# Kernel tuning notes

Measured on AMD Instinct MI355X. Metric: run time of the kernel, lower is better.

The kernel has to match this reference:

```python
import jax, jax.numpy as jnp
import numpy as np

N = 8192        # number of nodes (adjacency is N x N)
F_IN = 256      # in_features
F_OUT = 256     # out_features


def setup_inputs() -> dict:
    key = jax.random.key(0)
    k_x, k_adj, k_kernel, k_bias, k_beta = jax.random.split(key, 5)
    x = jax.random.normal(k_x, (N, F_IN), dtype=jnp.float32)
    adj = jax.random.uniform(k_adj, (N, N), dtype=jnp.float32)  # dense non-negative adjacency buffer
    # xavier-uniform-like scale for the kernel
    limit = float(np.sqrt(6.0 / (F_IN + F_OUT)))
    kernel = jax.random.uniform(k_kernel, (F_IN, F_OUT), dtype=jnp.float32, minval=-limit, maxval=limit)
    bias = 0.01 * jax.random.normal(k_bias, (F_OUT,), dtype=jnp.float32)
    beta = 0.01 * jax.random.normal(k_beta, (N,), dtype=jnp.float32)
    return {"x": x, "adj": adj, "kernel": kernel, "bias": bias, "beta": beta}


def reference(x, adj, kernel, bias, beta):
    # Original: diag(1/(rowsum(adj)+beta)) @ (adj + diag(beta)) @ x @ kernel + bias
    # Fused form: row-scale and diagonal-add applied without materializing NxN diag matrices.
    scale = jnp.reciprocal(jnp.sum(adj, axis=1) + beta)          # [N]
    agg = adj @ x + beta[:, None] * x                             # (adj + diag(beta)) @ x  -> [N, F_IN]
    return (scale[:, None] * agg) @ kernel + bias                 # [N, F_OUT]
```

## Files before the change

### kernel.cpp

```cpp
#include <hip/hip_runtime.h>
#include <hip/hip_bf16.h>


typedef __attribute__((ext_vector_type(8))) short  short8;
typedef __attribute__((ext_vector_type(4))) float  floatx4;

#define N_NODES 8192
#define F_DIM   256

#define ASYNC16(g, l)                                                          \
  __builtin_amdgcn_global_load_lds(                                           \
      (const __attribute__((address_space(1))) void*)(g),                     \
      (__attribute__((address_space(3))) void*)(l), 16, 0, 0)

__device__ __forceinline__ unsigned short f2bf(float f) {
  unsigned u = __float_as_uint(f);
  return (unsigned short)((u + 0x7FFFu + ((u >> 16) & 1u)) >> 16);
}

__device__ __forceinline__ short8 pack_bf16x8(floatx4 a, floatx4 b) {
  short8 r;
  r[0] = (short)f2bf(a.x);
  r[1] = (short)f2bf(a.y);
  r[2] = (short)f2bf(a.z);
  r[3] = (short)f2bf(a.w);
  r[4] = (short)f2bf(b.x);
  r[5] = (short)f2bf(b.y);
  r[6] = (short)f2bf(b.z);
  r[7] = (short)f2bf(b.w);
  return r;
}

__global__ __launch_bounds__(256) void tile_bf16_kernel(
    const float* __restrict__ src, unsigned short* __restrict__ dst, int K) {
  const int Nn = F_DIM;
  int cid = blockIdx.x * 256 + threadIdx.x;
  int per_kblk = Nn * 4;
  int kblk = cid / per_kblk;
  int rem  = cid - kblk * per_kblk;
  int n16 = rem >> 6;
  int kg  = (rem >> 4) & 3;
  int nl  = rem & 15;
  int n = n16 * 16 + nl;
  int k = kblk * 32 + kg * 8;
  const float* s = src + (size_t)k * Nn + n;
  floatx4 v0, v1;
  v0.x = s[0];
  v0.y = s[(size_t)Nn];
  v0.z = s[(size_t)2 * Nn];
  v0.w = s[(size_t)3 * Nn];
  v1.x = s[(size_t)4 * Nn];
  v1.y = s[(size_t)5 * Nn];
  v1.z = s[(size_t)6 * Nn];
  v1.w = s[(size_t)7 * Nn];
  *(short8*)(dst + (size_t)cid * 8) = pack_bf16x8(v0, v1);
}

template <int KS>
__global__ __launch_bounds__(256, 2) void stage1_kernel(
    const float* __restrict__ adj, const unsigned short* __restrict__ xbt,
    float* __restrict__ part, float* __restrict__ rsp) {
  __shared__ float         At[64 * 32];
  __shared__ unsigned short Bt[32 * F_DIM];

  const int tid = threadIdx.x;
  const int w  = tid >> 6;
  const int l  = tid & 63;
  const int kq = l >> 4;
  const int ml = l & 15;
  const int m0 = blockIdx.x * 64;
  const int ks = blockIdx.y;
  const int kbeg   = ks * (N_NODES / KS);
  const int KSTEPS = (N_NODES / KS) / 32;

  const int arow = w * 16 + (l >> 3);
  const int srcg = (l & 7) ^ ((l >> 3) & 7);
  const float* agp0 = adj + (size_t)(m0 + arow) * N_NODES + kbeg + srcg * 4;
  const float* agp1 = agp0 + (size_t)8 * N_NODES;
  float* aldst0 = At + (w * 2) * 256;
  float* aldst1 = At + (w * 2 + 1) * 256;
  const unsigned short* bgp =
      xbt + (size_t)(kbeg / 32) * (32 * F_DIM) + (w * 4) * 512 + l * 8;
  unsigned short* bldst = Bt + (w * 4) * 512;

  int aoff0[4], aoff1[4], boff[4];
#pragma unroll
  for (int mf = 0; mf < 4; ++mf) {
    int m = mf * 16 + ml;
    aoff0[mf] = m * 32 + (((kq * 2)     ^ (m & 7)) * 4);
    aoff1[mf] = m * 32 + (((kq * 2 + 1) ^ (m & 7)) * 4);
  }
#pragma unroll
  for (int nf = 0; nf < 4; ++nf)
    boff[nf] = (w * 4 + nf) * 512 + kq * 128 + ml * 8;

  floatx4 acc[4][4];
  const floatx4 zf4 = {0.f, 0.f, 0.f, 0.f};
#pragma unroll
  for (int mf = 0; mf < 4; ++mf)
#pragma unroll
    for (int nf = 0; nf < 4; ++nf) acc[mf][nf] = zf4;
  float rsum[4] = {0.f, 0.f, 0.f, 0.f};

  for (int s = 0; s < KSTEPS; ++s) {
    ASYNC16(agp0, aldst0);
    ASYNC16(agp1, aldst1);
    ASYNC16(bgp,         bldst);
    ASYNC16(bgp +  512,  bldst +  512);
    ASYNC16(bgp + 1024,  bldst + 1024);
    ASYNC16(bgp + 1536,  bldst + 1536);
    agp0 += 32; agp1 += 32; bgp += 32 * F_DIM;
    __syncthreads();

    short8 af[4];
#pragma unroll
    for (int mf = 0; mf < 4; ++mf) {
      floatx4 a0 = *(const floatx4*)(At + aoff0[mf]);
      floatx4 a1 = *(const floatx4*)(At + aoff1[mf]);
      if (w == 0)
        rsum[mf] += (a0.x + a0.y + a0.z + a0.w) + (a1.x + a1.y + a1.z + a1.w);
      af[mf] = pack_bf16x8(a0, a1);
    }
#pragma unroll
    for (int nf = 0; nf < 4; ++nf) {
      short8 bv = *(const short8*)(Bt + boff[nf]);
#pragma unroll
      for (int mf = 0; mf < 4; ++mf)
        acc[mf][nf] =
            __builtin_amdgcn_mfma_f32_16x16x32_bf16(af[mf], bv, acc[mf][nf], 0, 0, 0);
    }
    __syncthreads();
  }

  float* pout = part + (size_t)ks * N_NODES * F_DIM;
#pragma unroll
  for (int mf = 0; mf < 4; ++mf)
#pragma unroll
    for (int nf = 0; nf < 4; ++nf) {
      int col = w * 64 + nf * 16 + ml;
#pragma unroll
      for (int r = 0; r < 4; ++r) {
        int row = m0 + mf * 16 + kq * 4 + r;
        pout[(size_t)row * F_DIM + col] = acc[mf][nf][r];
      }
    }

  if (w == 0) {
#pragma unroll
    for (int mf = 0; mf < 4; ++mf) {
      float v = rsum[mf];
      v += __shfl_xor(v, 16);
      v += __shfl_xor(v, 32);
      if (kq == 0) rsp[ks * N_NODES + m0 + mf * 16 + ml] = v;
    }
  }
}

template <int KS>
__global__ __launch_bounds__(256, 2) void stage2_kernel(
    const float* part, const float* __restrict__ rsp,
    const float* __restrict__ x, const float* __restrict__ beta,
    const float* __restrict__ bias, const unsigned short* __restrict__ wbt,
    float* out) {
  __shared__ unsigned short At[32 * 32];
  __shared__ unsigned short Bt[32 * F_DIM];
  __shared__ float sscale[32];
  __shared__ float sbeta[32];

  const int tid = threadIdx.x;
  const int w  = tid >> 6;
  const int l  = tid & 63;
  const int kq = l >> 4;
  const int ml = l & 15;
  const int m0 = blockIdx.x * 32;

  if (tid < 32) {
    float rs = 0.f;
#pragma unroll
    for (int p = 0; p < KS; ++p) rs += rsp[p * N_NODES + m0 + tid];
    float b = beta[m0 + tid];
    sbeta[tid]  = b;
    sscale[tid] = 1.0f / (rs + b);
  }
  __syncthreads();

  floatx4 acc[2][4];
  const floatx4 zf4 = {0.f, 0.f, 0.f, 0.f};
#pragma unroll
  for (int mf = 0; mf < 2; ++mf)
#pragma unroll
    for (int nf = 0; nf < 4; ++nf) acc[mf][nf] = zf4;

  const unsigned short* bgp = wbt + (w * 4) * 512 + l * 8;
  unsigned short* bldst = Bt + (w * 4) * 512;

  for (int s = 0; s < 8; ++s) {
    ASYNC16(bgp,        bldst);
    ASYNC16(bgp +  512, bldst +  512);
    ASYNC16(bgp + 1024, bldst + 1024);
    ASYNC16(bgp + 1536, bldst + 1536);
    bgp += 32 * F_DIM;

    if (tid < 128) {
      int r = tid >> 2, g = tid & 3;
      size_t off = (size_t)(m0 + r) * F_DIM + s * 32 + g * 8;
      floatx4 v0 = *(const floatx4*)(x + off);
      floatx4 v1 = *(const floatx4*)(x + off + 4);
      float bb = sbeta[r];
      v0 *= bb; v1 *= bb;
#pragma unroll
      for (int p = 0; p < KS; ++p) {
        const float* pp = part + (size_t)p * N_NODES * F_DIM + off;
        v0 += *(const floatx4*)pp;
        v1 += *(const floatx4*)(pp + 4);
      }
      float sc = sscale[r];
      v0 *= sc; v1 *= sc;
      *(short8*)(At + r * 32 + ((g ^ (r & 3)) * 8)) = pack_bf16x8(v0, v1);
    }
    __syncthreads();

    short8 af[2];
#pragma unroll
    for (int mf = 0; mf < 2; ++mf) {
      int m = mf * 16 + ml;
      af[mf] = *(const short8*)(At + m * 32 + ((kq ^ (m & 3)) * 8));
    }
#pragma unroll
    for (int nf = 0; nf < 4; ++nf) {
      short8 bv = *(const short8*)(Bt + (w * 4 + nf) * 512 + kq * 128 + ml * 8);
#pragma unroll
      for (int mf = 0; mf < 2; ++mf)
        acc[mf][nf] =
            __builtin_amdgcn_mfma_f32_16x16x32_bf16(af[mf], bv, acc[mf][nf], 0, 0, 0);
    }
    __syncthreads();
  }

#pragma unroll
  for (int nf = 0; nf < 4; ++nf) {
    int col = w * 64 + nf * 16 + ml;
    float bv = bias[col];
#pragma unroll
    for (int mf = 0; mf < 2; ++mf)
#pragma unroll
      for (int r = 0; r < 4; ++r) {
        int row = m0 + mf * 16 + kq * 4 + r;
        out[(size_t)row * F_DIM + col] = acc[mf][nf][r] + bv;
      }
  }
}

extern "C" void kernel_launch(void* const* d_in, const int* in_sizes, int n_in,
                              void* d_out, int out_size, void* d_ws, size_t ws_size,
                              hipStream_t stream) {
  const float* x    = (const float*)d_in[0];
  const float* adj  = (const float*)d_in[1];
  const float* kern = (const float*)d_in[2];
  const float* bias = (const float*)d_in[3];
  const float* beta = (const float*)d_in[4];
  float* out = (float*)d_out;

  char* ws = (char*)d_ws;
  unsigned short* xbt = (unsigned short*)ws;
  unsigned short* wbt = xbt + (size_t)N_NODES * F_DIM;
  float* rsp  = (float*)(wbt + F_DIM * F_DIM);
  float* part = (float*)((char*)rsp + 4 * N_NODES * sizeof(float));

  const size_t base    = (size_t)N_NODES * F_DIM * 2 + (size_t)F_DIM * F_DIM * 2 +
                         4 * (size_t)N_NODES * 4;
  const size_t part_sz = (size_t)N_NODES * F_DIM * 4;

  tile_bf16_kernel<<<(N_NODES * F_DIM / 8) / 256, 256, 0, stream>>>(x, xbt, N_NODES);
  tile_bf16_kernel<<<(F_DIM * F_DIM / 8) / 256, 256, 0, stream>>>(kern, wbt, F_DIM);

  if (ws_size >= base + 4 * part_sz) {
    stage1_kernel<4><<<dim3(128, 4), 256, 0, stream>>>(adj, xbt, part, rsp);
    stage2_kernel<4><<<256, 256, 0, stream>>>(part, rsp, x, beta, bias, wbt, out);
  } else if (ws_size >= base + 2 * part_sz) {
    stage1_kernel<2><<<dim3(128, 2), 256, 0, stream>>>(adj, xbt, part, rsp);
    stage2_kernel<2><<<256, 256, 0, stream>>>(part, rsp, x, beta, bias, wbt, out);
  } else {
    stage1_kernel<1><<<dim3(128, 1), 256, 0, stream>>>(adj, xbt, out, rsp);
    stage2_kernel<1><<<256, 256, 0, stream>>>(out, rsp, x, beta, bias, wbt, out);
  }
}
```

Before: 439.9 us.

## Deepen stage1 K step to 64, raise split-K to 8, spread stage2 loads

```diff
diff --git a/kernel.cpp b/kernel.cpp
--- a/kernel.cpp
+++ b/kernel.cpp
@@ -3,6 +3,7 @@
 
 
 typedef __attribute__((ext_vector_type(8))) short  short8;
+typedef __attribute__((ext_vector_type(4))) short  short4v;
 typedef __attribute__((ext_vector_type(4))) float  floatx4;
 
 #define N_NODES 8192
@@ -20,14 +21,10 @@
 
 __device__ __forceinline__ short8 pack_bf16x8(floatx4 a, floatx4 b) {
   short8 r;
-  r[0] = (short)f2bf(a.x);
-  r[1] = (short)f2bf(a.y);
-  r[2] = (short)f2bf(a.z);
-  r[3] = (short)f2bf(a.w);
-  r[4] = (short)f2bf(b.x);
-  r[5] = (short)f2bf(b.y);
-  r[6] = (short)f2bf(b.z);
-  r[7] = (short)f2bf(b.w);
+  r[0] = (short)f2bf(a.x); r[1] = (short)f2bf(a.y);
+  r[2] = (short)f2bf(a.z); r[3] = (short)f2bf(a.w);
+  r[4] = (short)f2bf(b.x); r[5] = (short)f2bf(b.y);
+  r[6] = (short)f2bf(b.z); r[7] = (short)f2bf(b.w);
   return r;
 }
 
@@ -57,11 +54,11 @@
 }
 
 template <int KS>
-__global__ __launch_bounds__(256, 2) void stage1_kernel(
+__global__ __launch_bounds__(256, 3) void stage1_kernel(
     const float* __restrict__ adj, const unsigned short* __restrict__ xbt,
     float* __restrict__ part, float* __restrict__ rsp) {
-  __shared__ float         At[64 * 32];
-  __shared__ unsigned short Bt[32 * F_DIM];
+  __shared__ float          At[2][64 * 32];
+  __shared__ unsigned short Bt[64 * F_DIM];
 
   const int tid = threadIdx.x;
   const int w  = tid >> 6;
@@ -71,28 +68,27 @@
   const int m0 = blockIdx.x * 64;
   const int ks = blockIdx.y;
   const int kbeg   = ks * (N_NODES / KS);
-  const int KSTEPS = (N_NODES / KS) / 32;
+  const int KSTEPS = (N_NODES / KS) / 64;
 
   const int arow = w * 16 + (l >> 3);
   const int srcg = (l & 7) ^ ((l >> 3) & 7);
   const float* agp0 = adj + (size_t)(m0 + arow) * N_NODES + kbeg + srcg * 4;
   const float* agp1 = agp0 + (size_t)8 * N_NODES;
-  float* aldst0 = At + (w * 2) * 256;
-  float* aldst1 = At + (w * 2 + 1) * 256;
+  float* a0d0 = At[0] + (w * 2) * 256;
+  float* a0d1 = At[0] + (w * 2 + 1) * 256;
+  float* a1d0 = At[1] + (w * 2) * 256;
+  float* a1d1 = At[1] + (w * 2 + 1) * 256;
   const unsigned short* bgp =
-      xbt + (size_t)(kbeg / 32) * (32 * F_DIM) + (w * 4) * 512 + l * 8;
-  unsigned short* bldst = Bt + (w * 4) * 512;
-
-  int aoff0[4], aoff1[4], boff[4];
+      xbt + (size_t)(kbeg / 32) * (32 * F_DIM) + w * 4096 + l * 8;
+  unsigned short* bldst = Bt + w * 4096;
+
+  int aoff0[4], aoff1[4];
 #pragma unroll
   for (int mf = 0; mf < 4; ++mf) {
     int m = mf * 16 + ml;
     aoff0[mf] = m * 32 + (((kq * 2)     ^ (m & 7)) * 4);
     aoff1[mf] = m * 32 + (((kq * 2 + 1) ^ (m & 7)) * 4);
   }
-#pragma unroll
-  for (int nf = 0; nf < 4; ++nf)
-    boff[nf] = (w * 4 + nf) * 512 + kq * 128 + ml * 8;
 
   floatx4 acc[4][4];
   const floatx4 zf4 = {0.f, 0.f, 0.f, 0.f};
@@ -103,31 +99,35 @@
   float rsum[4] = {0.f, 0.f, 0.f, 0.f};
 
   for (int s = 0; s < KSTEPS; ++s) {
-    ASYNC16(agp0, aldst0);
-    ASYNC16(agp1, aldst1);
-    ASYNC16(bgp,         bldst);
-    ASYNC16(bgp +  512,  bldst +  512);
-    ASYNC16(bgp + 1024,  bldst + 1024);
-    ASYNC16(bgp + 1536,  bldst + 1536);
-    agp0 += 32; agp1 += 32; bgp += 32 * F_DIM;
-    __syncthreads();
-
-    short8 af[4];
-#pragma unroll
-    for (int mf = 0; mf < 4; ++mf) {
-      floatx4 a0 = *(const floatx4*)(At + aoff0[mf]);
-      floatx4 a1 = *(const floatx4*)(At + aoff1[mf]);
-      if (w == 0)
-        rsum[mf] += (a0.x + a0.y + a0.z + a0.w) + (a1.x + a1.y + a1.z + a1.w);
-      af[mf] = pack_bf16x8(a0, a1);
-    }
-#pragma unroll
-    for (int nf = 0; nf < 4; ++nf) {
-      short8 bv = *(const short8*)(Bt + boff[nf]);
-#pragma unroll
-      for (int mf = 0; mf < 4; ++mf)
-        acc[mf][nf] =
-            __builtin_amdgcn_mfma_f32_16x16x32_bf16(af[mf], bv, acc[mf][nf], 0, 0, 0);
+    ASYNC16(agp0,      a0d0);
+    ASYNC16(agp1,      a0d1);
+    ASYNC16(agp0 + 32, a1d0);
+    ASYNC16(agp1 + 32, a1d1);
+#pragma unroll
+    for (int i = 0; i < 8; ++i) ASYNC16(bgp + i * 512, bldst + i * 512);
+    agp0 += 64; agp1 += 64; bgp += 64 * F_DIM;
+    __syncthreads();
+
+#pragma unroll
+    for (int h = 0; h < 2; ++h) {
+      short8 af[4];
+#pragma unroll
+      for (int mf = 0; mf < 4; ++mf) {
+        floatx4 a0 = *(const floatx4*)(At[h] + aoff0[mf]);
+        floatx4 a1 = *(const floatx4*)(At[h] + aoff1[mf]);
+        if (w == 0)
+          rsum[mf] += (a0.x + a0.y + a0.z + a0.w) + (a1.x + a1.y + a1.z + a1.w);
+        af[mf] = pack_bf16x8(a0, a1);
+      }
+#pragma unroll
+      for (int nf = 0; nf < 4; ++nf) {
+        short8 bv = *(const short8*)(Bt + h * 8192 + (w * 4 + nf) * 512 +
+                                     kq * 128 + ml * 8);
+#pragma unroll
+        for (int mf = 0; mf < 4; ++mf)
+          acc[mf][nf] = __builtin_amdgcn_mfma_f32_16x16x32_bf16(
+              af[mf], bv, acc[mf][nf], 0, 0, 0);
+      }
     }
     __syncthreads();
   }
@@ -173,6 +173,8 @@
   const int kq = l >> 4;
   const int ml = l & 15;
   const int m0 = blockIdx.x * 32;
+  const int ar = tid >> 3;
+  const int ag = tid & 7;
 
   if (tid < 32) {
     float rs = 0.f;
@@ -193,6 +195,9 @@
 
   const unsigned short* bgp = wbt + (w * 4) * 512 + l * 8;
   unsigned short* bldst = Bt + (w * 4) * 512;
+  const float bb = sbeta[ar];
+  const float sc = sscale[ar];
+  unsigned short* adst = At + ar * 32 + (((ag >> 1) ^ (ar & 3)) * 8) + (ag & 1) * 4;
 
   for (int s = 0; s < 8; ++s) {
     ASYNC16(bgp,        bldst);
@@ -201,22 +206,17 @@
     ASYNC16(bgp + 1536, bldst + 1536);
     bgp += 32 * F_DIM;
 
-    if (tid < 128) {
-      int r = tid >> 2, g = tid & 3;
-      size_t off = (size_t)(m0 + r) * F_DIM + s * 32 + g * 8;
-      floatx4 v0 = *(const floatx4*)(x + off);
-      floatx4 v1 = *(const floatx4*)(x + off + 4);
-      float bb = sbeta[r];
-      v0 *= bb; v1 *= bb;
-#pragma unroll
-      for (int p = 0; p < KS; ++p) {
-        const float* pp = part + (size_t)p * N_NODES * F_DIM + off;
-        v0 += *(const floatx4*)pp;
-        v1 += *(const floatx4*)(pp + 4);
-      }
-      float sc = sscale[r];
-      v0 *= sc; v1 *= sc;
-      *(short8*)(At + r * 32 + ((g ^ (r & 3)) * 8)) = pack_bf16x8(v0, v1);
+    {
+      size_t off = (size_t)(m0 + ar) * F_DIM + s * 32 + ag * 4;
+      floatx4 v = *(const floatx4*)(x + off) * bb;
+#pragma unroll
+      for (int p = 0; p < KS; ++p)
+        v += *(const floatx4*)(part + (size_t)p * N_NODES * F_DIM + off);
+      v *= sc;
+      short4v pv;
+      pv[0] = (short)f2bf(v.x); pv[1] = (short)f2bf(v.y);
+      pv[2] = (short)f2bf(v.z); pv[3] = (short)f2bf(v.w);
+      *(short4v*)adst = pv;
     }
     __syncthreads();
 
@@ -265,21 +265,21 @@
   unsigned short* xbt = (unsigned short*)ws;
   unsigned short* wbt = xbt + (size_t)N_NODES * F_DIM;
   float* rsp  = (float*)(wbt + F_DIM * F_DIM);
-  float* part = (float*)((char*)rsp + 4 * N_NODES * sizeof(float));
+  float* part = (float*)((char*)rsp + 8 * N_NODES * sizeof(float));
 
   const size_t base    = (size_t)N_NODES * F_DIM * 2 + (size_t)F_DIM * F_DIM * 2 +
-                         4 * (size_t)N_NODES * 4;
+                         8 * (size_t)N_NODES * 4;
   const size_t part_sz = (size_t)N_NODES * F_DIM * 4;
 
   tile_bf16_kernel<<<(N_NODES * F_DIM / 8) / 256, 256, 0, stream>>>(x, xbt, N_NODES);
   tile_bf16_kernel<<<(F_DIM * F_DIM / 8) / 256, 256, 0, stream>>>(kern, wbt, F_DIM);
 
-  if (ws_size >= base + 4 * part_sz) {
+  if (ws_size >= base + 8 * part_sz) {
+    stage1_kernel<8><<<dim3(128, 8), 256, 0, stream>>>(adj, xbt, part, rsp);
+    stage2_kernel<8><<<256, 256, 0, stream>>>(part, rsp, x, beta, bias, wbt, out);
+  } else if (ws_size >= base + 4 * part_sz) {
     stage1_kernel<4><<<dim3(128, 4), 256, 0, stream>>>(adj, xbt, part, rsp);
     stage2_kernel<4><<<256, 256, 0, stream>>>(part, rsp, x, beta, bias, wbt, out);
-  } else if (ws_size >= base + 2 * part_sz) {
-    stage1_kernel<2><<<dim3(128, 2), 256, 0, stream>>>(adj, xbt, part, rsp);
-    stage2_kernel<2><<<256, 256, 0, stream>>>(part, rsp, x, beta, bias, wbt, out);
   } else {
     stage1_kernel<1><<<dim3(128, 1), 256, 0, stream>>>(adj, xbt, out, rsp);
     stage2_kernel<1><<<256, 256, 0, stream>>>(out, rsp, x, beta, bias, wbt, out);
```

Measured after the change: 457.7 us. +4.0%, slower.
